# Optimization experiments

Hardware: AMD Instinct MI355X
Metric: run time of the kernel (lower is better)

Reference implementation:

```python
import jax, jax.numpy as jnp
import numpy as np

N_NODES = 100000
N_EDGES = 1600000
IN_DIM, HID_DIM, OUT_DIM = 128, 64, 64
NEG_SLOPE = 0.2


def _gat_layer(h_in, src, dst, W, a_src, a_dst, b, n_nodes):
    # h: [N, F_out]
    h = h_in @ W.T
    alpha_src = h @ a_src  # [N]
    alpha_dst = h @ a_dst  # [N]
    # per-edge raw attention logits (edge j->i: src=j, dst=i)
    e = jax.nn.leaky_relu(alpha_src[src] + alpha_dst[dst], NEG_SLOPE)  # [E]
    # segment softmax over incoming edges of each dst node
    m = jax.ops.segment_max(e, dst, num_segments=n_nodes)
    ex = jnp.exp(e - m[dst])
    denom = jax.ops.segment_sum(ex, dst, num_segments=n_nodes)
    alpha = ex / denom[dst]  # [E], denom > 0 thanks to self-loops
    out = jax.ops.segment_sum(h[src] * alpha[:, None], dst, num_segments=n_nodes)
    return out + b


def setup_inputs() -> dict:
    key = jax.random.key(0)
    ks = jax.random.split(key, 12)
    x = jax.random.normal(ks[0], (N_NODES, IN_DIM), dtype=jnp.float32)
    edge_index = jax.random.randint(ks[1], (2, N_EDGES), 0, N_NODES)
    edge_attr = jax.random.normal(ks[2], (N_EDGES, 1), dtype=jnp.float32)
    s1 = 1.0 / np.sqrt(IN_DIM)
    s2 = 1.0 / np.sqrt(HID_DIM)
    W1 = jax.random.normal(ks[3], (HID_DIM, IN_DIM), dtype=jnp.float32) * s1
    att_src1 = jax.random.normal(ks[4], (HID_DIM,), dtype=jnp.float32) * s2
    att_dst1 = jax.random.normal(ks[5], (HID_DIM,), dtype=jnp.float32) * s2
    b1 = jnp.zeros((HID_DIM,), dtype=jnp.float32)
    W2 = jax.random.normal(ks[6], (OUT_DIM, HID_DIM), dtype=jnp.float32) * s2
    att_src2 = jax.random.normal(ks[7], (OUT_DIM,), dtype=jnp.float32) * s2
    att_dst2 = jax.random.normal(ks[8], (OUT_DIM,), dtype=jnp.float32) * s2
    b2 = jnp.zeros((OUT_DIM,), dtype=jnp.float32)
    return {"x": x, "edge_index": edge_index, "edge_attr": edge_attr,
            "W1": W1, "att_src1": att_src1, "att_dst1": att_dst1, "b1": b1,
            "W2": W2, "att_src2": att_src2, "att_dst2": att_dst2, "b2": b2}


def reference(x, edge_index, edge_attr, W1, att_src1, att_dst1, b1,
              W2, att_src2, att_dst2, b2):
    n = x.shape[0]
    # add self-loops (PyG GATConv default); edge_attr unused (edge_dim=None)
    loop = jnp.arange(n, dtype=edge_index.dtype)
    src = jnp.concatenate([edge_index[0], loop])
    dst = jnp.concatenate([edge_index[1], loop])
    h = _gat_layer(x, src, dst, W1, att_src1, att_dst1, b1, n)
    h = jax.nn.relu(h)
    h = _gat_layer(h, src, dst, W2, att_src2, att_dst2, b2, n)
    # global_mean_pool with batch=None -> mean over all nodes, shape [1, F]
    return jnp.mean(h, axis=0, keepdims=True)
```

## Files before the change

### kernel.cpp

```cpp
#include <hip/hip_runtime.h>

#define NEG_SLOPE 0.2f
#define BSHIFT 6
#define NBMAX 2048
#define BCAP 1408
#define CHUNK 4096

typedef __attribute__((ext_vector_type(8))) short short8;
typedef __attribute__((ext_vector_type(4))) float f32x4;

__device__ __forceinline__ unsigned short f2b(float x) {
    unsigned u = __float_as_uint(x);
    u += 0x7fff + ((u >> 16) & 1);
    return (unsigned short)(u >> 16);
}
__device__ __forceinline__ float b2f(unsigned short u) {
    return __uint_as_float((unsigned)u << 16);
}

__global__ __launch_bounds__(256) void hist_kernel(
    const int* __restrict__ ei, int* __restrict__ hist, int E, int NB)
{
    __shared__ int cnt[NBMAX];
    const int tid = threadIdx.x;
    for (int i = tid; i < NB; i += 256) cnt[i] = 0;
    __syncthreads();
    const int start = blockIdx.x * CHUNK;
    const int end = min(start + CHUNK, E);
    for (int i = start + tid; i < end; i += 256)
        atomicAdd(&cnt[ei[E + i] >> BSHIFT], 1);
    __syncthreads();
    for (int i = tid; i < NB; i += 256)
        hist[(size_t)blockIdx.x * NB + i] = cnt[i];
}

__global__ __launch_bounds__(256) void colscan_kernel(
    int* __restrict__ hist, int* __restrict__ btotal, int NB, int NBLK)
{
    const int b = blockIdx.x * 256 + threadIdx.x;
    if (b >= NB) return;
    int run = 0;
    int blk = 0;
    for (; blk + 8 <= NBLK; blk += 8) {
        int w[8];
        #pragma unroll
        for (int j = 0; j < 8; ++j) w[j] = hist[(size_t)(blk + j) * NB + b];
        #pragma unroll
        for (int j = 0; j < 8; ++j) {
            hist[(size_t)(blk + j) * NB + b] = run;
            run += w[j];
        }
    }
    for (; blk < NBLK; ++blk) {
        int w = hist[(size_t)blk * NB + b];
        hist[(size_t)blk * NB + b] = run;
        run += w;
    }
    btotal[b] = run;
}

__global__ __launch_bounds__(256) void scatter_kernel(
    const int* __restrict__ ei, const int* __restrict__ hist,
    int* __restrict__ binned, int E, int NB)
{
    __shared__ int base[NBMAX], cnt2[NBMAX];
    const int tid = threadIdx.x;
    for (int i = tid; i < NB; i += 256) {
        base[i] = hist[(size_t)blockIdx.x * NB + i];
        cnt2[i] = 0;
    }
    __syncthreads();
    const int start = blockIdx.x * CHUNK;
    const int end = min(start + CHUNK, E);
    for (int i = start + tid; i < end; i += 256) {
        int s = ei[i], d = ei[E + i];
        int b = d >> BSHIFT;
        int r = base[b] + atomicAdd(&cnt2[b], 1);
        if (r < BCAP) binned[(size_t)b * BCAP + r] = (s << BSHIFT) | (d & 63);
    }
}

__global__ __launch_bounds__(256) void bscan_kernel(
    const int* __restrict__ btotal, int* __restrict__ bbase, int NB)
{
    __shared__ int lds[256];
    const int t = threadIdx.x;
    int v[8]; int s = 0;
    #pragma unroll
    for (int j = 0; j < 8; ++j) {
        int i = t * 8 + j;
        v[j] = (i < NB) ? min(btotal[i], BCAP) : 0;
        s += v[j];
    }
    lds[t] = s;
    __syncthreads();
    #pragma unroll
    for (int off = 1; off < 256; off <<= 1) {
        int x = (t >= off) ? lds[t - off] : 0;
        __syncthreads();
        lds[t] += x;
        __syncthreads();
    }
    int excl = (t > 0) ? lds[t - 1] : 0;
    #pragma unroll
    for (int j = 0; j < 8; ++j) {
        int i = t * 8 + j;
        if (i < NB) { bbase[i] = excl + 64 * i; excl += v[j]; }
    }
}

__global__ __launch_bounds__(256) void bucket_csr_kernel(
    const int* __restrict__ binned, const int* __restrict__ btotal,
    const int* __restrict__ bbase, int* __restrict__ row_ptr,
    int* __restrict__ esrc, int N)
{
    __shared__ int ldeg[64];
    __shared__ int lcur[64];
    const int b = blockIdx.x;
    const int tid = threadIdx.x;
    const int node0 = b << BSHIFT;
    const int cnt = min(btotal[b], BCAP);
    const int base_e = bbase[b];
    const int* bp = binned + (size_t)b * BCAP;

    if (tid < 64) ldeg[tid] = (node0 + tid < N) ? 1 : 0;
    __syncthreads();
    for (int i = tid; i < cnt; i += 256)
        atomicAdd(&ldeg[bp[i] & 63], 1);
    __syncthreads();
    if (tid < 64) {
        int v = ldeg[tid];
        int inc = v;
        #pragma unroll
        for (int off = 1; off < 64; off <<= 1) {
            int t2 = __shfl_up(inc, off, 64);
            if (tid >= off) inc += t2;
        }
        int excl = inc - v;
        int node = node0 + tid;
        if (node <= N) row_ptr[node] = base_e + excl;
        if (node < N) {
            esrc[base_e + excl] = node;
            lcur[tid] = base_e + excl + 1;
        }
    }
    __syncthreads();
    for (int i = tid; i < cnt; i += 256) {
        int v = bp[i];
        int pos = atomicAdd(&lcur[v & 63], 1);
        esrc[pos] = v >> BSHIFT;
    }
}

template<int K, bool BF16IN>
__global__ __launch_bounds__(256) void gemm_attn_kernel(
    const void* __restrict__ in_v, const float* __restrict__ W,
    const float* __restrict__ a_src, const float* __restrict__ a_dst,
    unsigned short* __restrict__ hb, float* __restrict__ asrc,
    float* __restrict__ adst, int N)
{
    constexpr int LDK = K + 8;
    __shared__ unsigned short xb[64 * LDK];
    __shared__ unsigned short wb[64 * LDK];
    __shared__ float avs[64], avd[64];

    const int tid = threadIdx.x;
    const int node0 = blockIdx.x * 64;
    const int w = tid >> 6;
    const int lane = tid & 63;
    const int col = lane & 15;
    const int quad = lane >> 4;

    if (tid < 64) { avs[tid] = a_src[tid]; avd[tid] = a_dst[tid]; }

    for (int i = tid; i < 64 * (K / 4); i += 256) {
        int r = i / (K / 4), c = i % (K / 4);
        float4 v = *(const float4*)&W[(size_t)r * K + 4 * c];
        *(ushort4*)&wb[r * LDK + 4 * c] =
            make_ushort4(f2b(v.x), f2b(v.y), f2b(v.z), f2b(v.w));
    }
    if (BF16IN) {
        const unsigned short* in = (const unsigned short*)in_v;
        for (int i = tid; i < 64 * (K / 8); i += 256) {
            int r = i / (K / 8), c = i % (K / 8);
            int node = node0 + r;
            ulonglong2 v = (node < N)
                ? *(const ulonglong2*)&in[(size_t)node * K + 8 * c]
                : make_ulonglong2(0ull, 0ull);
            *(ulonglong2*)&xb[r * LDK + 8 * c] = v;
        }
    } else {
        const float* in = (const float*)in_v;
        for (int i = tid; i < 64 * (K / 4); i += 256) {
            int r = i / (K / 4), c = i % (K / 4);
            int node = node0 + r;
            float4 v = (node < N) ? *(const float4*)&in[(size_t)node * K + 4 * c]
                                  : make_float4(0.f, 0.f, 0.f, 0.f);
            *(ushort4*)&xb[r * LDK + 4 * c] =
                make_ushort4(f2b(v.x), f2b(v.y), f2b(v.z), f2b(v.w));
        }
    }
    __syncthreads();

    f32x4 acc[4] = {f32x4{0,0,0,0}, f32x4{0,0,0,0}, f32x4{0,0,0,0}, f32x4{0,0,0,0}};
    #pragma unroll
    for (int kc = 0; kc < K / 32; ++kc) {
        short8 a = *(const short8*)&xb[(16 * w + col) * LDK + kc * 32 + quad * 8];
        #pragma unroll
        for (int j = 0; j < 4; ++j) {
            short8 b = *(const short8*)&wb[(16 * j + col) * LDK + kc * 32 + quad * 8];
            acc[j] = __builtin_amdgcn_mfma_f32_16x16x32_bf16(a, b, acc[j], 0, 0, 0);
        }
    }

    #pragma unroll
    for (int r = 0; r < 4; ++r) {
        const int node = node0 + 16 * w + quad * 4 + r;
        const bool valid = node < N;
        float vs = 0.f, vd = 0.f;
        #pragma unroll
        for (int j = 0; j < 4; ++j) {
            float hv = acc[j][r];
            int f = 16 * j + col;
            if (valid) hb[(size_t)node * 64 + f] = f2b(hv);
            vs = fmaf(hv, avs[f], vs);
            vd = fmaf(hv, avd[f], vd);
        }
        #pragma unroll
        for (int off = 8; off >= 1; off >>= 1) {
            vs += __shfl_down(vs, off, 16);
            vd += __shfl_down(vd, off, 16);
        }
        if (col == 0 && valid) { asrc[node] = vs; adst[node] = vd; }
    }
}

__global__ __launch_bounds__(256) void aggregate_csr_kernel(
    const int* __restrict__ row_ptr, const int* __restrict__ esrc,
    const float* __restrict__ asrc, const float* __restrict__ adst,
    const unsigned short* __restrict__ hb, const float* __restrict__ bias,
    unsigned short* __restrict__ gb, int N, int do_relu)
{
    const int node = (int)((blockIdx.x * 256 + threadIdx.x) >> 4);
    const int lane = threadIdx.x & 15;
    if (node >= N) return;
    const int beg = row_ptr[node];
    const int end = row_ptr[node + 1];
    const float ad = adst[node];
    float a0 = 0.f, a1 = 0.f, a2 = 0.f, a3 = 0.f, wsum = 0.f;
    int p = beg;
    for (; p + 4 <= end; p += 4) {
        int s[4]; ushort4 r[4]; float l[4];
        #pragma unroll
        for (int j = 0; j < 4; ++j) s[j] = esrc[p + j];
        #pragma unroll
        for (int j = 0; j < 4; ++j)
            r[j] = *(const ushort4*)(hb + (size_t)s[j] * 64 + lane * 4);
        #pragma unroll
        for (int j = 0; j < 4; ++j) l[j] = asrc[s[j]] + ad;
        #pragma unroll
        for (int j = 0; j < 4; ++j) {
            float ll = (l[j] > 0.f) ? l[j] : NEG_SLOPE * l[j];
            float w = __expf(ll);
            wsum += w;
            a0 = fmaf(w, b2f(r[j].x), a0);
            a1 = fmaf(w, b2f(r[j].y), a1);
            a2 = fmaf(w, b2f(r[j].z), a2);
            a3 = fmaf(w, b2f(r[j].w), a3);
        }
    }
    for (; p < end; ++p) {
        int s = esrc[p];
        ushort4 r = *(const ushort4*)(hb + (size_t)s * 64 + lane * 4);
        float l = asrc[s] + ad;
        l = (l > 0.f) ? l : NEG_SLOPE * l;
        float w = __expf(l);
        wsum += w;
        a0 = fmaf(w, b2f(r.x), a0);
        a1 = fmaf(w, b2f(r.y), a1);
        a2 = fmaf(w, b2f(r.z), a2);
        a3 = fmaf(w, b2f(r.w), a3);
    }
    const float inv = 1.0f / wsum;
    float4 v = make_float4(a0 * inv, a1 * inv, a2 * inv, a3 * inv);
    if (bias) {
        v.x += bias[lane * 4 + 0]; v.y += bias[lane * 4 + 1];
        v.z += bias[lane * 4 + 2]; v.w += bias[lane * 4 + 3];
    }
    if (do_relu) {
        v.x = fmaxf(v.x, 0.f); v.y = fmaxf(v.y, 0.f);
        v.z = fmaxf(v.z, 0.f); v.w = fmaxf(v.w, 0.f);
    }
    *(ushort4*)&gb[(size_t)node * 64 + lane * 4] =
        make_ushort4(f2b(v.x), f2b(v.y), f2b(v.z), f2b(v.w));
}

__global__ __launch_bounds__(256) void pool_kernel(
    const unsigned short* __restrict__ gb, const float* __restrict__ b2,
    float* __restrict__ out, int N)
{
    __shared__ float red[256];
    const int f = threadIdx.x & 63;
    const int sub = threadIdx.x >> 6;
    float acc = 0.f;
    for (int n = blockIdx.x * 4 + sub; n < N; n += gridDim.x * 4)
        acc += b2f(gb[(size_t)n * 64 + f]);
    red[threadIdx.x] = acc;
    __syncthreads();
    if (threadIdx.x < 64) {
        float s = red[f] + red[64 + f] + red[128 + f] + red[192 + f];
        atomicAdd(out + f, s * (1.0f / (float)N));
        if (blockIdx.x == 0) atomicAdd(out + f, b2[f]);
    }
}

extern "C" void kernel_launch(void* const* d_in, const int* in_sizes, int n_in,
                              void* d_out, int out_size, void* d_ws, size_t ws_size,
                              hipStream_t stream) {
    const float* x   = (const float*)d_in[0];
    const int*   ei  = (const int*)d_in[1];
    const float* W1  = (const float*)d_in[3];
    const float* as1 = (const float*)d_in[4];
    const float* ad1 = (const float*)d_in[5];
    const float* b1  = (const float*)d_in[6];
    const float* W2  = (const float*)d_in[7];
    const float* as2 = (const float*)d_in[8];
    const float* ad2 = (const float*)d_in[9];
    const float* b2  = (const float*)d_in[10];
    float* out = (float*)d_out;

    const int N = in_sizes[0] / 128;
    const int E = in_sizes[1] / 2;
    const int Etot = E + N;
    const int NB = (N + 63) >> BSHIFT;
    const int NBLK = (E + CHUNK - 1) / CHUNK;

    auto align4 = [](size_t v) { return (v + 3) & ~(size_t)3; };
    float* ws    = (float*)d_ws;
    size_t off = 0;
    unsigned short* hb = (unsigned short*)(ws + off); off += align4((size_t)N * 32);
    unsigned short* gb = (unsigned short*)(ws + off); off += align4((size_t)N * 32);
    float* asrc  = ws + off; off += align4(N);
    float* adst  = ws + off; off += align4(N);
    int* row_ptr = (int*)(ws + off); off += align4(N + 1);
    int* btotal  = (int*)(ws + off); off += NBMAX;
    int* bbase   = (int*)(ws + off); off += NBMAX;
    int* hist    = (int*)(ws + off); off += align4((size_t)NBLK * NB);
    int* esrc    = (int*)(ws + off); off += align4(Etot);
    int* binned  = (int*)gb;

    const int gemm_blocks = (N + 63) / 64;
    const int agg_blocks  = (int)(((size_t)N * 16 + 255) / 256);

    hipMemsetAsync(out, 0, 64 * sizeof(float), stream);

    hist_kernel<<<NBLK, 256, 0, stream>>>(ei, hist, E, NB);
    colscan_kernel<<<(NB + 255) / 256, 256, 0, stream>>>(hist, btotal, NB, NBLK);
    scatter_kernel<<<NBLK, 256, 0, stream>>>(ei, hist, binned, E, NB);
    bscan_kernel<<<1, 256, 0, stream>>>(btotal, bbase, NB);
    bucket_csr_kernel<<<NB, 256, 0, stream>>>(binned, btotal, bbase, row_ptr, esrc, N);

    gemm_attn_kernel<128, false><<<gemm_blocks, 256, 0, stream>>>(
        x, W1, as1, ad1, hb, asrc, adst, N);
    aggregate_csr_kernel<<<agg_blocks, 256, 0, stream>>>(
        row_ptr, esrc, asrc, adst, hb, b1, gb, N, 1);

    gemm_attn_kernel<64, true><<<gemm_blocks, 256, 0, stream>>>(
        gb, W2, as2, ad2, hb, asrc, adst, N);
    aggregate_csr_kernel<<<agg_blocks, 256, 0, stream>>>(
        row_ptr, esrc, asrc, adst, hb, nullptr, gb, N, 0);

    pool_kernel<<<512, 256, 0, stream>>>(gb, b2, out, N);
}
```

Before: 298.4 us.

## Fuse pooling into final aggregate, drop bucket scan, pre-convert weights

Removes the single-block bucket scan by giving each bucket a fixed stride in the edge array, storing separate row begin and end arrays. Weights are converted to bf16 once in a small kernel instead of in every GEMM block. The second aggregation writes per-block partial sums through LDS atomics rather than storing the bf16 output for a separate pool pass, and the aggregation loop is unrolled to 8 edges. The cost is a padded edge array, LDS atomic contention in the pooled path, and an extra launch for the weight conversion.

```diff
diff --git a/kernel.cpp b/kernel.cpp
--- a/kernel.cpp
+++ b/kernel.cpp
@@ -4,6 +4,7 @@
 #define BSHIFT 6
 #define NBMAX 2048
 #define BCAP 1408
+#define ESTRIDE (BCAP + 64)
 #define CHUNK 4096
 
 typedef __attribute__((ext_vector_type(8))) short short8;
@@ -16,6 +17,15 @@
 }
 __device__ __forceinline__ float b2f(unsigned short u) {
     return __uint_as_float((unsigned)u << 16);
+}
+
+__global__ __launch_bounds__(256) void wconv_kernel(
+    const float* __restrict__ W1, const float* __restrict__ W2,
+    unsigned short* __restrict__ wb1, unsigned short* __restrict__ wb2)
+{
+    int i = blockIdx.x * 256 + threadIdx.x;
+    if (i < 64 * 128) wb1[i] = f2b(W1[i]);
+    else if (i < 64 * 128 + 64 * 64) wb2[i - 8192] = f2b(W2[i - 8192]);
 }
 
 __global__ __launch_bounds__(256) void hist_kernel(
@@ -80,38 +90,9 @@
     }
 }
 
-__global__ __launch_bounds__(256) void bscan_kernel(
-    const int* __restrict__ btotal, int* __restrict__ bbase, int NB)
-{
-    __shared__ int lds[256];
-    const int t = threadIdx.x;
-    int v[8]; int s = 0;
-    #pragma unroll
-    for (int j = 0; j < 8; ++j) {
-        int i = t * 8 + j;
-        v[j] = (i < NB) ? min(btotal[i], BCAP) : 0;
-        s += v[j];
-    }
-    lds[t] = s;
-    __syncthreads();
-    #pragma unroll
-    for (int off = 1; off < 256; off <<= 1) {
-        int x = (t >= off) ? lds[t - off] : 0;
-        __syncthreads();
-        lds[t] += x;
-        __syncthreads();
-    }
-    int excl = (t > 0) ? lds[t - 1] : 0;
-    #pragma unroll
-    for (int j = 0; j < 8; ++j) {
-        int i = t * 8 + j;
-        if (i < NB) { bbase[i] = excl + 64 * i; excl += v[j]; }
-    }
-}
-
 __global__ __launch_bounds__(256) void bucket_csr_kernel(
     const int* __restrict__ binned, const int* __restrict__ btotal,
-    const int* __restrict__ bbase, int* __restrict__ row_ptr,
+    int* __restrict__ row_beg, int* __restrict__ row_end,
     int* __restrict__ esrc, int N)
 {
     __shared__ int ldeg[64];
@@ -120,7 +101,7 @@
     const int tid = threadIdx.x;
     const int node0 = b << BSHIFT;
     const int cnt = min(btotal[b], BCAP);
-    const int base_e = bbase[b];
+    const int base_e = b * ESTRIDE;
     const int* bp = binned + (size_t)b * BCAP;
 
     if (tid < 64) ldeg[tid] = (node0 + tid < N) ? 1 : 0;
@@ -138,8 +119,9 @@
         }
         int excl = inc - v;
         int node = node0 + tid;
-        if (node <= N) row_ptr[node] = base_e + excl;
         if (node < N) {
+            row_beg[node] = base_e + excl;
+            row_end[node] = base_e + inc;
             esrc[base_e + excl] = node;
             lcur[tid] = base_e + excl + 1;
         }
@@ -154,7 +136,7 @@
 
 template<int K, bool BF16IN>
 __global__ __launch_bounds__(256) void gemm_attn_kernel(
-    const void* __restrict__ in_v, const float* __restrict__ W,
+    const void* __restrict__ in_v, const unsigned short* __restrict__ Wb,
     const float* __restrict__ a_src, const float* __restrict__ a_dst,
     unsigned short* __restrict__ hb, float* __restrict__ asrc,
     float* __restrict__ adst, int N)
@@ -173,11 +155,9 @@
 
     if (tid < 64) { avs[tid] = a_src[tid]; avd[tid] = a_dst[tid]; }
 
-    for (int i = tid; i < 64 * (K / 4); i += 256) {
-        int r = i / (K / 4), c = i % (K / 4);
-        float4 v = *(const float4*)&W[(size_t)r * K + 4 * c];
-        *(ushort4*)&wb[r * LDK + 4 * c] =
-            make_ushort4(f2b(v.x), f2b(v.y), f2b(v.z), f2b(v.w));
+    for (int i = tid; i < 64 * (K / 8); i += 256) {
+        int r = i / (K / 8), c = i % (K / 8);
+        *(ulonglong2*)&wb[r * LDK + 8 * c] = *(const ulonglong2*)&Wb[(size_t)r * K + 8 * c];
     }
     if (BF16IN) {
         const unsigned short* in = (const unsigned short*)in_v;
@@ -235,76 +215,94 @@
     }
 }
 
+template<bool POOL>
 __global__ __launch_bounds__(256) void aggregate_csr_kernel(
-    const int* __restrict__ row_ptr, const int* __restrict__ esrc,
+    const int* __restrict__ row_beg, const int* __restrict__ row_end,
+    const int* __restrict__ esrc,
     const float* __restrict__ asrc, const float* __restrict__ adst,
     const unsigned short* __restrict__ hb, const float* __restrict__ bias,
-    unsigned short* __restrict__ gb, int N, int do_relu)
-{
+    unsigned short* __restrict__ gb, float* __restrict__ partials, int N)
+{
+    __shared__ float psum[64];
+    if (POOL) {
+        if (threadIdx.x < 64) psum[threadIdx.x] = 0.f;
+        __syncthreads();
+    }
     const int node = (int)((blockIdx.x * 256 + threadIdx.x) >> 4);
     const int lane = threadIdx.x & 15;
-    if (node >= N) return;
-    const int beg = row_ptr[node];
-    const int end = row_ptr[node + 1];
-    const float ad = adst[node];
-    float a0 = 0.f, a1 = 0.f, a2 = 0.f, a3 = 0.f, wsum = 0.f;
-    int p = beg;
-    for (; p + 4 <= end; p += 4) {
-        int s[4]; ushort4 r[4]; float l[4];
-        #pragma unroll
-        for (int j = 0; j < 4; ++j) s[j] = esrc[p + j];
-        #pragma unroll
-        for (int j = 0; j < 4; ++j)
-            r[j] = *(const ushort4*)(hb + (size_t)s[j] * 64 + lane * 4);
-        #pragma unroll
-        for (int j = 0; j < 4; ++j) l[j] = asrc[s[j]] + ad;
-        #pragma unroll
-        for (int j = 0; j < 4; ++j) {
-            float ll = (l[j] > 0.f) ? l[j] : NEG_SLOPE * l[j];
-            float w = __expf(ll);
+    if (node < N) {
+        const int beg = row_beg[node];
+        const int end = row_end[node];
+        const float ad = adst[node];
+        float a0 = 0.f, a1 = 0.f, a2 = 0.f, a3 = 0.f, wsum = 0.f;
+        int p = beg;
+        for (; p + 8 <= end; p += 8) {
+            int s[8]; ushort4 r[8]; float l[8];
+            #pragma unroll
+            for (int j = 0; j < 8; ++j) s[j] = esrc[p + j];
+            #pragma unroll
+            for (int j = 0; j < 8; ++j)
+                r[j] = *(const ushort4*)(hb + (size_t)s[j] * 64 + lane * 4);
+            #pragma unroll
+            for (int j = 0; j < 8; ++j) l[j] = asrc[s[j]] + ad;
+            #pragma unroll
+            for (int j = 0; j < 8; ++j) {
+                float ll = (l[j] > 0.f) ? l[j] : NEG_SLOPE * l[j];
+                float w = __expf(ll);
+                wsum += w;
+                a0 = fmaf(w, b2f(r[j].x), a0);
+                a1 = fmaf(w, b2f(r[j].y), a1);
+                a2 = fmaf(w, b2f(r[j].z), a2);
+                a3 = fmaf(w, b2f(r[j].w), a3);
+            }
+        }
+        for (; p < end; ++p) {
+            int s = esrc[p];
+            ushort4 r = *(const ushort4*)(hb + (size_t)s * 64 + lane * 4);
+            float l = asrc[s] + ad;
+            l = (l > 0.f) ? l : NEG_SLOPE * l;
+            float w = __expf(l);
             wsum += w;
-            a0 = fmaf(w, b2f(r[j].x), a0);
-            a1 = fmaf(w, b2f(r[j].y), a1);
-            a2 = fmaf(w, b2f(r[j].z), a2);
-            a3 = fmaf(w, b2f(r[j].w), a3);
-        }
-    }
-    for (; p < end; ++p) {
-        int s = esrc[p];
-        ushort4 r = *(const ushort4*)(hb + (size_t)s * 64 + lane * 4);
-        float l = asrc[s] + ad;
-        l = (l > 0.f) ? l : NEG_SLOPE * l;
-        float w = __expf(l);
-        wsum += w;
-        a0 = fmaf(w, b2f(r.x), a0);
-        a1 = fmaf(w, b2f(r.y), a1);
-        a2 = fmaf(w, b2f(r.z), a2);
-        a3 = fmaf(w, b2f(r.w), a3);
-    }
-    const float inv = 1.0f / wsum;
-    float4 v = make_float4(a0 * inv, a1 * inv, a2 * inv, a3 * inv);
-    if (bias) {
-        v.x += bias[lane * 4 + 0]; v.y += bias[lane * 4 + 1];
-        v.z += bias[lane * 4 + 2]; v.w += bias[lane * 4 + 3];
-    }
-    if (do_relu) {
-        v.x = fmaxf(v.x, 0.f); v.y = fmaxf(v.y, 0.f);
-        v.z = fmaxf(v.z, 0.f); v.w = fmaxf(v.w, 0.f);
-    }
-    *(ushort4*)&gb[(size_t)node * 64 + lane * 4] =
-        make_ushort4(f2b(v.x), f2b(v.y), f2b(v.z), f2b(v.w));
-}
-
-__global__ __launch_bounds__(256) void pool_kernel(
-    const unsigned short* __restrict__ gb, const float* __restrict__ b2,
-    float* __restrict__ out, int N)
+            a0 = fmaf(w, b2f(r.x), a0);
+            a1 = fmaf(w, b2f(r.y), a1);
+            a2 = fmaf(w, b2f(r.z), a2);
+            a3 = fmaf(w, b2f(r.w), a3);
+        }
+        const float inv = 1.0f / wsum;
+        float4 v = make_float4(a0 * inv, a1 * inv, a2 * inv, a3 * inv);
+        if (!POOL) {
+            if (bias) {
+                v.x += bias[lane * 4 + 0]; v.y += bias[lane * 4 + 1];
+                v.z += bias[lane * 4 + 2]; v.w += bias[lane * 4 + 3];
+            }
+            v.x = fmaxf(v.x, 0.f); v.y = fmaxf(v.y, 0.f);
+            v.z = fmaxf(v.z, 0.f); v.w = fmaxf(v.w, 0.f);
+            *(ushort4*)&gb[(size_t)node * 64 + lane * 4] =
+                make_ushort4(f2b(v.x), f2b(v.y), f2b(v.z), f2b(v.w));
+        } else {
+            atomicAdd(&psum[lane * 4 + 0], v.x);
+            atomicAdd(&psum[lane * 4 + 1], v.y);
+            atomicAdd(&psum[lane * 4 + 2], v.z);
+            atomicAdd(&psum[lane * 4 + 3], v.w);
+        }
+    }
+    if (POOL) {
+        __syncthreads();
+        if (threadIdx.x < 64)
+            partials[(size_t)blockIdx.x * 64 + threadIdx.x] = psum[threadIdx.x];
+    }
+}
+
+__global__ __launch_bounds__(256) void pool_final_kernel(
+    const float* __restrict__ partials, const float* __restrict__ b2,
+    float* __restrict__ out, int nblk, int N)
 {
     __shared__ float red[256];
     const int f = threadIdx.x & 63;
     const int sub = threadIdx.x >> 6;
     float acc = 0.f;
-    for (int n = blockIdx.x * 4 + sub; n < N; n += gridDim.x * 4)
-        acc += b2f(gb[(size_t)n * 64 + f]);
+    for (int r = blockIdx.x * 4 + sub; r < nblk; r += gridDim.x * 4)
+        acc += partials[(size_t)r * 64 + f];
     red[threadIdx.x] = acc;
     __syncthreads();
     if (threadIdx.x < 64) {
@@ -331,9 +329,9 @@
 
     const int N = in_sizes[0] / 128;
     const int E = in_sizes[1] / 2;
-    const int Etot = E + N;
     const int NB = (N + 63) >> BSHIFT;
     const int NBLK = (E + CHUNK - 1) / CHUNK;
+    const int agg_blocks = (int)(((size_t)N * 16 + 255) / 256);
 
     auto align4 = [](size_t v) { return (v + 3) & ~(size_t)3; };
     float* ws    = (float*)d_ws;
@@ -342,33 +340,35 @@
     unsigned short* gb = (unsigned short*)(ws + off); off += align4((size_t)N * 32);
     float* asrc  = ws + off; off += align4(N);
     float* adst  = ws + off; off += align4(N);
-    int* row_ptr = (int*)(ws + off); off += align4(N + 1);
+    int* row_beg = (int*)(ws + off); off += align4(N);
+    int* row_end = (int*)(ws + off); off += align4(N);
     int* btotal  = (int*)(ws + off); off += NBMAX;
-    int* bbase   = (int*)(ws + off); off += NBMAX;
+    unsigned short* wb1 = (unsigned short*)(ws + off); off += align4(64 * 128 / 2);
+    unsigned short* wb2 = (unsigned short*)(ws + off); off += align4(64 * 64 / 2);
+    float* partials = ws + off; off += align4((size_t)agg_blocks * 64);
     int* hist    = (int*)(ws + off); off += align4((size_t)NBLK * NB);
-    int* esrc    = (int*)(ws + off); off += align4(Etot);
+    int* esrc    = (int*)(ws + off); off += align4((size_t)NB * ESTRIDE);
     int* binned  = (int*)gb;
 
     const int gemm_blocks = (N + 63) / 64;
-    const int agg_blocks  = (int)(((size_t)N * 16 + 255) / 256);
 
     hipMemsetAsync(out, 0, 64 * sizeof(float), stream);
+    wconv_kernel<<<48, 256, 0, stream>>>(W1, W2, wb1, wb2);
 
     hist_kernel<<<NBLK, 256, 0, stream>>>(ei, hist, E, NB);
     colscan_kernel<<<(NB + 255) / 256, 256, 0, stream>>>(hist, btotal, NB, NBLK);
     scatter_kernel<<<NBLK, 256, 0, stream>>>(ei, hist, binned, E, NB);
-    bscan_kernel<<<1, 256, 0, stream>>>(btotal, bbase, NB);
-    bucket_csr_kernel<<<NB, 256, 0, stream>>>(binned, btotal, bbase, row_ptr, esrc, N);
+    bucket_csr_kernel<<<NB, 256, 0, stream>>>(binned, btotal, row_beg, row_end, esrc, N);
 
     gemm_attn_kernel<128, false><<<gemm_blocks, 256, 0, stream>>>(
-        x, W1, as1, ad1, hb, asrc, adst, N);
-    aggregate_csr_kernel<<<agg_blocks, 256, 0, stream>>>(
-        row_ptr, esrc, asrc, adst, hb, b1, gb, N, 1);
+        x, wb1, as1, ad1, hb, asrc, adst, N);
+    aggregate_csr_kernel<false><<<agg_blocks, 256, 0, stream>>>(
+        row_beg, row_end, esrc, asrc, adst, hb, b1, gb, nullptr, N);
 
     gemm_attn_kernel<64, true><<<gemm_blocks, 256, 0, stream>>>(
-        gb, W2, as2, ad2, hb, asrc, adst, N);
-    aggregate_csr_kernel<<<agg_blocks, 256, 0, stream>>>(
-        row_ptr, esrc, asrc, adst, hb, nullptr, gb, N, 0);
-
-    pool_kernel<<<512, 256, 0, stream>>>(gb, b2, out, N);
-}
+        gb, wb2, as2, ad2, hb, asrc, adst, N);
+    aggregate_csr_kernel<true><<<agg_blocks, 256, 0, stream>>>(
+        row_beg, row_end, esrc, asrc, adst, hb, nullptr, nullptr, partials, N);
+
+    pool_final_kernel<<<64, 256, 0, stream>>>(partials, b2, out, agg_blocks, N);
+}
```

Result: slower. 309.0 us (+3.5%).
